# Kernel optimization log

Measured on AMD Instinct MI355X. Metric: run time of the kernel, lower is better.

Reference implementation:

```python
import jax, jax.numpy as jnp
import numpy as np

B, T, D, H = 4, 1024, 1024, 16
DS, DC, EXP = 16, 4, 2
DI = EXP * D            # 2048 inner SSM dim
DTR = D // 16           # 64 dt rank
K = max(1, int(0.2 * T))  # top-k tokens routed to attention
HD = D // H


def setup_inputs() -> dict:
    key = jax.random.key(0)
    ks = jax.random.split(key, 12)
    s = 0.02
    w = lambda k, shp: jax.random.normal(k, shp, jnp.float32) * s
    return {
        "x": jax.random.normal(ks[0], (B, T, D), jnp.float32),
        "ln_gamma": jnp.ones((D,), jnp.float32),
        "ln_beta": jnp.zeros((D,), jnp.float32),
        "Wr1": w(ks[1], (D, D // 4)), "br1": jnp.zeros((D // 4,), jnp.float32),
        "Wr2": w(ks[2], (D // 4, 1)), "br2": jnp.zeros((1,), jnp.float32),
        "Wqkv": w(ks[3], (D, 3 * D)), "bqkv": jnp.zeros((3 * D,), jnp.float32),
        "Wo": w(ks[4], (D, D)), "bo": jnp.zeros((D,), jnp.float32),
        "W_in": w(ks[5], (D, 2 * DI)),
        "conv_w": w(ks[6], (DI, DC)), "conv_b": jnp.zeros((DI,), jnp.float32),
        "W_xproj": w(ks[7], (DI, DTR + 2 * DS)),
        "W_dt": w(ks[8], (DTR, DI)), "b_dt": jnp.zeros((DI,), jnp.float32),
        "A_log": jnp.log(jnp.broadcast_to(jnp.arange(1, DS + 1, dtype=jnp.float32), (DI, DS))),
        "Dskip": jnp.ones((DI,), jnp.float32),
        "W_out": w(ks[9], (DI, D)),
    }


def _layernorm(x, g, b):
    mu = x.mean(-1, keepdims=True)
    v = ((x - mu) ** 2).mean(-1, keepdims=True)
    return (x - mu) * jax.lax.rsqrt(v + 1e-5) * g + b


def _attn(tok, Wqkv, bqkv, Wo, bo):
    # full MHA over the k selected tokens only: tok (B,K,D)
    qkv = tok @ Wqkv + bqkv
    q, k_, v = jnp.split(qkv, 3, axis=-1)
    q = q.reshape(B, K, H, HD).transpose(0, 2, 1, 3)   # bhkd
    k_ = k_.reshape(B, K, H, HD).transpose(0, 2, 1, 3)
    v = v.reshape(B, K, H, HD).transpose(0, 2, 1, 3)
    scores = jnp.einsum('bhqd,bhkd->bhqk', q, k_) / jnp.sqrt(jnp.float32(HD))
    p = jax.nn.softmax(scores, axis=-1)
    o = jnp.einsum('bhqk,bhkd->bhqd', p, v)
    o = o.transpose(0, 2, 1, 3).reshape(B, K, D)
    return o @ Wo + bo


def _ssm(xn, W_in, conv_w, conv_b, W_xproj, W_dt, b_dt, A_log, Dskip, W_out):
    # Mamba-style selective SSM over all tokens
    u, z = jnp.split(xn @ W_in, 2, axis=-1)            # (B,T,DI) each
    up = jnp.pad(u, ((0, 0), (DC - 1, 0), (0, 0)))      # causal depthwise conv
    uc = sum(up[:, j:j + T, :] * conv_w[:, j] for j in range(DC)) + conv_b
    u = jax.nn.silu(uc)
    proj = u @ W_xproj                                  # (B,T,DTR+2*DS)
    dt = jax.nn.softplus(proj[..., :DTR] @ W_dt + b_dt)  # (B,T,DI)
    Bm = proj[..., DTR:DTR + DS]                        # (B,T,DS)
    Cm = proj[..., DTR + DS:]                           # (B,T,DS)
    A = -jnp.exp(A_log)                                 # (DI,DS)
    dA = jnp.exp(dt[..., None] * A)                     # (B,T,DI,DS)
    dBu = dt[..., None] * Bm[:, :, None, :] * u[..., None]

    def step(h, inp):
        dA_t, dBu_t, C_t = inp
        h = dA_t * h + dBu_t                            # (B,DI,DS)
        y = (h * C_t[:, None, :]).sum(-1)               # (B,DI)
        return h, y

    h0 = jnp.zeros((B, DI, DS), dA.dtype)
    _, ys = jax.lax.scan(step, h0, (dA.transpose(1, 0, 2, 3),
                                    dBu.transpose(1, 0, 2, 3),
                                    Cm.transpose(1, 0, 2)))
    y = ys.transpose(1, 0, 2) + u * Dskip               # (B,T,DI)
    y = y * jax.nn.silu(z)
    return y @ W_out


def reference(x, ln_gamma, ln_beta, Wr1, br1, Wr2, br2, Wqkv, bqkv, Wo, bo,
              W_in, conv_w, conv_b, W_xproj, W_dt, b_dt, A_log, Dskip, W_out):
    xn = _layernorm(x, ln_gamma, ln_beta)
    scores = (jax.nn.relu(xn @ Wr1 + br1) @ Wr2 + br2)[..., 0]   # (B,T)
    _, idx = jax.lax.top_k(scores, K)                            # (B,K)
    bidx = jnp.arange(B)[:, None]
    mask = jnp.zeros((B, T), bool).at[bidx, idx].set(True)
    delta_ssm = _ssm(xn, W_in, conv_w, conv_b, W_xproj, W_dt, b_dt, A_log, Dskip, W_out)
    tok = xn[bidx, idx]                                          # gather (B,K,D)
    delta_tok = _attn(tok, Wqkv, bqkv, Wo, bo)
    delta_attn = jnp.zeros_like(xn).at[bidx, idx].set(delta_tok)  # scatter back
    delta = jnp.where(mask[..., None], delta_attn, delta_ssm)
    return x + delta
```

## Files before the change

kernel.cpp:

```cpp
#include <hip/hip_runtime.h>
#include <hip/hip_bf16.h>
#include <math.h>

#define BB   4
#define TT   1024
#define DD   1024
#define HH   16
#define DII  2048
#define DSS  16
#define DCC  4
#define KK   204
#define HDD  64
#define DTRR 64
#define NCH  32
#define LCH  32
#define KSPL 8
#define XPN  96
#define PRJ  128
#define RZ   8
#define RKC  3072
#define MPAD 896
#define WOZ  4

typedef short bf16x8 __attribute__((ext_vector_type(8)));
typedef short bf16x4v __attribute__((ext_vector_type(4)));
typedef float f32x4 __attribute__((ext_vector_type(4)));

#define GLDS16(g, l) __builtin_amdgcn_global_load_lds(                        \
    (const __attribute__((address_space(1))) void*)(g),                       \
    (__attribute__((address_space(3))) void*)(l), 16, 0, 0)

__device__ __forceinline__ ushort f2bu(float v) {
  __hip_bfloat16 h = __float2bfloat16(v);
  return __builtin_bit_cast(ushort, h);
}
__device__ __forceinline__ float b2f(ushort u) {
  __hip_bfloat16 h = __builtin_bit_cast(__hip_bfloat16, u);
  return __bfloat162float(h);
}

__device__ __forceinline__ float wave_sum(float v) {
#pragma unroll
  for (int o = 32; o > 0; o >>= 1) v += __shfl_xor(v, o, 64);
  return v;
}
__device__ __forceinline__ float block_sum256(float v, volatile float* sh) {
  v = wave_sum(v);
  if ((threadIdx.x & 63) == 0) sh[threadIdx.x >> 6] = v;
  __syncthreads();
  float r = sh[0] + sh[1] + sh[2] + sh[3];
  __syncthreads();
  return r;
}

__global__ __launch_bounds__(256) void layernorm_kernel(
    const float* __restrict__ x, const float* __restrict__ g,
    const float* __restrict__ be, ushort* __restrict__ xcat) {
  __shared__ float sh[4];
  int row = blockIdx.x;
  const float* xr = x + (size_t)row * DD;
  float v[4];
  float s = 0.f;
#pragma unroll
  for (int i = 0; i < 4; i++) { v[i] = xr[threadIdx.x + 256 * i]; s += v[i]; }
  float mean = block_sum256(s, sh) * (1.f / DD);
  float q = 0.f;
#pragma unroll
  for (int i = 0; i < 4; i++) { float d = v[i] - mean; q += d * d; }
  float var = block_sum256(q, sh) * (1.f / DD);
  float rstd = rsqrtf(var + 1e-5f);
  ushort* xc = xcat + (size_t)row * RKC;
#pragma unroll
  for (int i = 0; i < 4; i++) {
    int c = threadIdx.x + 256 * i;
    float o = (v[i] - mean) * rstd * g[c] + be[c];
    ushort hi = f2bu(o);
    float lo = o - b2f(hi);
    xc[c] = hi;
    xc[1024 + c] = hi;
    xc[2048 + c] = f2bu(lo);
  }
}

__device__ __forceinline__ void tile_transpose(
    const float* W, int rows, int cols, ushort* WT, int bx, int by,
    float tile[32][33]) {
  int c0 = bx * 32, r0 = by * 32;
  int tx = threadIdx.x & 31, ty = threadIdx.x >> 5;
#pragma unroll
  for (int i = 0; i < 32; i += 8)
    tile[ty + i][tx] = W[(size_t)(r0 + ty + i) * cols + c0 + tx];
  __syncthreads();
#pragma unroll
  for (int i = 0; i < 32; i += 8)
    WT[(size_t)(c0 + ty + i) * rows + r0 + tx] = f2bu(tile[tx][ty + i]);
}

__global__ __launch_bounds__(256) void transpose_all(
    const float* __restrict__ W_in, const float* __restrict__ W_out,
    const float* __restrict__ Wqkv, const float* __restrict__ Wo,
    const float* __restrict__ W_dt, const float* __restrict__ W_xproj,
    ushort* __restrict__ WinT, ushort* __restrict__ WoutT,
    ushort* __restrict__ WqkvT, ushort* __restrict__ WoT,
    ushort* __restrict__ WdtT, ushort* __restrict__ WxprojT) {
  __shared__ float tile[32][33];
  int lin = blockIdx.x;
  if (lin < 4096) {
    tile_transpose(W_in, 1024, 4096, WinT, lin % 128, lin / 128, tile);
  } else if ((lin -= 4096) < 2048) {
    tile_transpose(W_out, 2048, 1024, WoutT, lin % 32, lin / 32, tile);
  } else if ((lin -= 2048) < 3072) {
    tile_transpose(Wqkv, 1024, 3072, WqkvT, lin % 96, lin / 96, tile);
  } else if ((lin -= 3072) < 1024) {
    tile_transpose(Wo, 1024, 1024, WoT, lin % 32, lin / 32, tile);
  } else if ((lin -= 1024) < 128) {
    tile_transpose(W_dt, 64, 2048, WdtT, lin % 64, lin / 64, tile);
  } else {
    lin -= 128;
    tile_transpose(W_xproj, 2048, 96, WxprojT, lin % 3, lin / 3, tile);
  }
}

__global__ __launch_bounds__(256) void transpose_hilo(
    const float* __restrict__ W, ushort* __restrict__ WT) {
  __shared__ float tile[32][33];
  int c0 = blockIdx.x * 32, r0 = blockIdx.y * 32;
  int tx = threadIdx.x & 31, ty = threadIdx.x >> 5;
#pragma unroll
  for (int i = 0; i < 32; i += 8)
    tile[ty + i][tx] = W[(size_t)(r0 + ty + i) * 256 + c0 + tx];
  __syncthreads();
#pragma unroll
  for (int i = 0; i < 32; i += 8) {
    float v = tile[tx][ty + i];
    ushort hi = f2bu(v);
    float lo = v - b2f(hi);
    size_t base = (size_t)(c0 + ty + i) * RKC;
    WT[base + r0 + tx] = hi;
    WT[base + 1024 + r0 + tx] = f2bu(lo);
    WT[base + 2048 + r0 + tx] = hi;
  }
}

__global__ __launch_bounds__(512) void gemm_bf16_256(
    const ushort* __restrict__ A, int lda,
    const ushort* __restrict__ BT, int ldbt,
    void* __restrict__ Cv, int ldc, int K,
    const float* __restrict__ bias, const float* __restrict__ addmat,
    int outBf16) {
  __shared__ ushort Alds[256 * 64];
  __shared__ ushort Blds[256 * 64];
  int t = threadIdx.x;
  int wv = t >> 6, lane = t & 63;
  int wvm = wv >> 2, wvn = wv & 3;
  int nwg = gridDim.x * gridDim.y;
  int lin = blockIdx.y * gridDim.x + blockIdx.x;
  int swz = (lin & 7) * (nwg >> 3) + (lin >> 3);
  int bx = swz % gridDim.x, by = swz / gridDim.x;
  int row0 = by * 256, col0 = bx * 256;
  f32x4 acc[8][4] = {};

  const ushort* Ap[4];
  const ushort* Bp[4];
  ushort* Alb[4];
  ushort* Blb[4];
#pragma unroll
  for (int j = 0; j < 4; j++) {
    int c = j * 512 + t;
    int r = c >> 3;
    int kc = (((c & 7) ^ (r & 7)) * 8);
    Ap[j] = A + (size_t)(row0 + r) * lda + kc;
    Bp[j] = BT + (size_t)(col0 + r) * ldbt + kc;
    int cst = j * 512 + wv * 64;
    Alb[j] = Alds + (size_t)cst * 8;
    Blb[j] = Blds + (size_t)cst * 8;
  }
  int frow = lane & 15, fk = (lane >> 4) * 8;

  for (int k0 = 0; k0 < K; k0 += 64) {
#pragma unroll
    for (int j = 0; j < 4; j++) {
      GLDS16(Ap[j] + k0, Alb[j]);
      GLDS16(Bp[j] + k0, Blb[j]);
    }
    __syncthreads();
#pragma unroll
    for (int ks = 0; ks < 2; ks++) {
      bf16x8 af[8], bfv[4];
#pragma unroll
      for (int m = 0; m < 8; m++) {
        int row = wvm * 128 + m * 16 + frow;
        af[m] = *(const bf16x8*)&Alds[row * 64 +
                                      ((ks * 32 + fk) ^ ((row & 7) * 8))];
      }
#pragma unroll
      for (int n = 0; n < 4; n++) {
        int row = wvn * 64 + n * 16 + frow;
        bfv[n] = *(const bf16x8*)&Blds[row * 64 +
                                       ((ks * 32 + fk) ^ ((row & 7) * 8))];
      }
#pragma unroll
      for (int m = 0; m < 8; m++)
#pragma unroll
        for (int n = 0; n < 4; n++)
          acc[m][n] = __builtin_amdgcn_mfma_f32_16x16x32_bf16(af[m], bfv[n],
                                                              acc[m][n], 0, 0, 0);
    }
    __syncthreads();
  }
  int rbase = row0 + wvm * 128 + (lane >> 4) * 4;
  int cbase = col0 + wvn * 64 + (lane & 15);
  if (outBf16) {
    ushort* myL = Alds + wv * 1088;
    ushort* C16 = (ushort*)Cv;
    for (int m = 0; m < 8; m++) {
      __syncthreads();
#pragma unroll
      for (int n = 0; n < 4; n++) {
        int cc = cbase + n * 16;
        float bi = bias ? bias[cc] : 0.f;
#pragma unroll
        for (int i = 0; i < 4; i++)
          myL[((lane >> 4) * 4 + i) * 68 + (lane & 15) + n * 16] =
              f2bu(acc[m][n][i] + bi);
      }
      __syncthreads();
      int rr = lane >> 2, cg = lane & 3;
      bf16x8 v0 = *(const bf16x8*)&myL[rr * 68 + cg * 16];
      bf16x8 v1 = *(const bf16x8*)&myL[rr * 68 + cg * 16 + 8];
      size_t grow = (size_t)(row0 + wvm * 128 + m * 16 + rr) * ldc +
                    col0 + wvn * 64 + cg * 16;
      *(bf16x8*)&C16[grow] = v0;
      *(bf16x8*)&C16[grow + 8] = v1;
    }
  } else {
    float* C = (float*)Cv;
#pragma unroll
    for (int n = 0; n < 4; n++) {
      int cc = cbase + n * 16;
      float bi = bias ? bias[cc] : 0.f;
#pragma unroll
      for (int m = 0; m < 8; m++) {
#pragma unroll
        for (int i = 0; i < 4; i++) {
          size_t r = rbase + m * 16 + i;
          float v = acc[m][n][i] + bi;
          if (addmat) v += addmat[r * ldc + cc];
          C[r * ldc + cc] = v;
        }
      }
    }
  }
}

__global__ __launch_bounds__(512) void gemm_bf16_128x8(
    const ushort* __restrict__ A, int lda,
    const ushort* __restrict__ BT, int ldbt,
    void* __restrict__ Cv, int ldc, int K,
    const float* __restrict__ bias, const float* __restrict__ addmat,
    int act, int outBf16) {
  __shared__ ushort Alds[128 * 64];
  __shared__ ushort Blds[128 * 64];
  int t = threadIdx.x;
  int wv = t >> 6, lane = t & 63;
  int wvm = wv >> 1, wvn = wv & 1;
  int nwg = gridDim.x * gridDim.y;
  int lin = blockIdx.y * gridDim.x + blockIdx.x;
  int swz = (lin & 7) * (nwg >> 3) + (lin >> 3);
  int bx = swz % gridDim.x, by = swz / gridDim.x;
  int row0 = by * 128, col0 = bx * 128;
  f32x4 acc[2][4] = {};

  const ushort* Ap[2];
  const ushort* Bp[2];
  ushort* Alb[2];
  ushort* Blb[2];
#pragma unroll
  for (int j = 0; j < 2; j++) {
    int c = j * 512 + t;
    int r = c >> 3;
    int kc = (((c & 7) ^ (r & 7)) * 8);
    Ap[j] = A + (size_t)(row0 + r) * lda + kc;
    Bp[j] = BT + (size_t)(col0 + r) * ldbt + kc;
    int cst = j * 512 + wv * 64;
    Alb[j] = Alds + (size_t)cst * 8;
    Blb[j] = Blds + (size_t)cst * 8;
  }
  int frow = lane & 15, fk = (lane >> 4) * 8;

  for (int k0 = 0; k0 < K; k0 += 64) {
#pragma unroll
    for (int j = 0; j < 2; j++) {
      GLDS16(Ap[j] + k0, Alb[j]);
      GLDS16(Bp[j] + k0, Blb[j]);
    }
    __syncthreads();
#pragma unroll
    for (int ks = 0; ks < 2; ks++) {
      bf16x8 af[2], bfv[4];
#pragma unroll
      for (int m = 0; m < 2; m++) {
        int row = wvm * 32 + m * 16 + frow;
        af[m] = *(const bf16x8*)&Alds[row * 64 +
                                      ((ks * 32 + fk) ^ ((row & 7) * 8))];
      }
#pragma unroll
      for (int n = 0; n < 4; n++) {
        int row = wvn * 64 + n * 16 + frow;
        bfv[n] = *(const bf16x8*)&Blds[row * 64 +
                                       ((ks * 32 + fk) ^ ((row & 7) * 8))];
      }
#pragma unroll
      for (int m = 0; m < 2; m++)
#pragma unroll
        for (int n = 0; n < 4; n++)
          acc[m][n] = __builtin_amdgcn_mfma_f32_16x16x32_bf16(af[m], bfv[n],
                                                              acc[m][n], 0, 0, 0);
    }
    __syncthreads();
  }
  int rbase = row0 + wvm * 32 + (lane >> 4) * 4;
  int cbase = col0 + wvn * 64 + (lane & 15);
#pragma unroll
  for (int n = 0; n < 4; n++) {
    int cc = cbase + n * 16;
    float bi = bias ? bias[cc] : 0.f;
#pragma unroll
    for (int m = 0; m < 2; m++) {
#pragma unroll
      for (int i = 0; i < 4; i++) {
        size_t r = rbase + m * 16 + i;
        float v = acc[m][n][i] + bi;
        if (act == 2) v = (v > 20.f) ? v : log1pf(__expf(v));
        if (outBf16) {
          ((ushort*)Cv)[r * ldc + cc] = f2bu(v);
        } else {
          if (addmat) v += addmat[r * ldc + cc];
          ((float*)Cv)[r * ldc + cc] = v;
        }
      }
    }
  }
}

__global__ __launch_bounds__(512) void gemm_bf16_128x8_splitk(
    const ushort* __restrict__ A, int lda,
    const ushort* __restrict__ BT, int ldbt,
    float* __restrict__ partial, int ldc, int Ktot, size_t zstride) {
  __shared__ ushort Alds[128 * 64];
  __shared__ ushort Blds[128 * 64];
  int t = threadIdx.x;
  int wv = t >> 6, lane = t & 63;
  int wvm = wv >> 1, wvn = wv & 1;
  int nwg = gridDim.x * gridDim.y;
  int lin = blockIdx.y * gridDim.x + blockIdx.x;
  int swz = (lin & 7) * (nwg >> 3) + (lin >> 3);
  int bx = swz % gridDim.x, by = swz / gridDim.x;
  int row0 = by * 128, col0 = bx * 128;
  int kchunk = Ktot / gridDim.z;
  int kbeg = blockIdx.z * kchunk, kend = kbeg + kchunk;
  f32x4 acc[2][4] = {};

  const ushort* Ap[2];
  const ushort* Bp[2];
  ushort* Alb[2];
  ushort* Blb[2];
#pragma unroll
  for (int j = 0; j < 2; j++) {
    int c = j * 512 + t;
    int r = c >> 3;
    int kc = (((c & 7) ^ (r & 7)) * 8);
    Ap[j] = A + (size_t)(row0 + r) * lda + kc;
    Bp[j] = BT + (size_t)(col0 + r) * ldbt + kc;
    int cst = j * 512 + wv * 64;
    Alb[j] = Alds + (size_t)cst * 8;
    Blb[j] = Blds + (size_t)cst * 8;
  }
  int frow = lane & 15, fk = (lane >> 4) * 8;

  for (int k0 = kbeg; k0 < kend; k0 += 64) {
#pragma unroll
    for (int j = 0; j < 2; j++) {
      GLDS16(Ap[j] + k0, Alb[j]);
      GLDS16(Bp[j] + k0, Blb[j]);
    }
    __syncthreads();
#pragma unroll
    for (int ks = 0; ks < 2; ks++) {
      bf16x8 af[2], bfv[4];
#pragma unroll
      for (int m = 0; m < 2; m++) {
        int row = wvm * 32 + m * 16 + frow;
        af[m] = *(const bf16x8*)&Alds[row * 64 +
                                      ((ks * 32 + fk) ^ ((row & 7) * 8))];
      }
#pragma unroll
      for (int n = 0; n < 4; n++) {
        int row = wvn * 64 + n * 16 + frow;
        bfv[n] = *(const bf16x8*)&Blds[row * 64 +
                                       ((ks * 32 + fk) ^ ((row & 7) * 8))];
      }
#pragma unroll
      for (int m = 0; m < 2; m++)
#pragma unroll
        for (int n = 0; n < 4; n++)
          acc[m][n] = __builtin_amdgcn_mfma_f32_16x16x32_bf16(af[m], bfv[n],
                                                              acc[m][n], 0, 0, 0);
    }
    __syncthreads();
  }
  float* P = partial + (size_t)blockIdx.z * zstride;
  int rbase = row0 + wvm * 32 + (lane >> 4) * 4;
  int cbase = col0 + wvn * 64 + (lane & 15);
#pragma unroll
  for (int n = 0; n < 4; n++) {
    int cc = cbase + n * 16;
#pragma unroll
    for (int m = 0; m < 2; m++)
#pragma unroll
      for (int i = 0; i < 4; i++)
        P[(size_t)(rbase + m * 16 + i) * ldc + cc] = acc[m][n][i];
  }
}

__global__ __launch_bounds__(256) void router_score_reduce(
    const float* __restrict__ rpart, const float* __restrict__ br1,
    const float* __restrict__ Wr2, const float* __restrict__ br2,
    float* __restrict__ scores, size_t zstride) {
  __shared__ float sh[4];
  int row = blockIdx.x, c = threadIdx.x;
  size_t idx = (size_t)row * 256 + c;
  float s = 0.f;
#pragma unroll
  for (int z = 0; z < RZ; z++) s += rpart[z * zstride + idx];
  s = fmaxf(s + br1[c], 0.f);
  float tot = block_sum256(s * Wr2[c], sh);
  if (c == 0) scores[row] = tot + br2[0];
}

__global__ __launch_bounds__(256) void wo_scatter_reduce(
    const float* __restrict__ wpart, const float* __restrict__ x,
    const float* __restrict__ bo, const int* __restrict__ idx,
    float* __restrict__ out, size_t zstride) {
  int r = blockIdx.x;
  int b = r / KK;
  size_t orow = (size_t)(b * TT + idx[r]) * DD;
  int c4 = threadIdx.x * 4;
  f32x4 s = *(const f32x4*)&wpart[(size_t)r * DD + c4];
#pragma unroll
  for (int z = 1; z < WOZ; z++) {
    f32x4 p = *(const f32x4*)&wpart[z * zstride + (size_t)r * DD + c4];
#pragma unroll
    for (int j = 0; j < 4; j++) s[j] += p[j];
  }
  f32x4 xv = *(const f32x4*)&x[orow + c4];
  f32x4 bv = *(const f32x4*)&bo[c4];
#pragma unroll
  for (int j = 0; j < 4; j++) s[j] += xv[j] + bv[j];
  *(f32x4*)&out[orow + c4] = s;
}

__global__ __launch_bounds__(1024) void topk_kernel(
    const float* __restrict__ scores, int* __restrict__ idx) {
  __shared__ float s[1024];
  __shared__ int si[1024];
  int b = blockIdx.x, t = threadIdx.x;
  s[t] = scores[b * TT + t];
  si[t] = t;
  __syncthreads();
  for (int k = 2; k <= 1024; k <<= 1) {
    for (int j = k >> 1; j > 0; j >>= 1) {
      int partner = t ^ j;
      if (partner > t) {
        bool dirDesc = ((t & k) == 0);
        float s1 = s[t], s2 = s[partner];
        int i1 = si[t], i2 = si[partner];
        bool firstGreater = (s1 > s2) || (s1 == s2 && i1 < i2);
        bool doSwap = dirDesc ? !firstGreater : firstGreater;
        if (doSwap) { s[t] = s2; s[partner] = s1; si[t] = i2; si[partner] = i1; }
      }
      __syncthreads();
    }
  }
  if (t < KK) idx[b * KK + t] = si[t];
}

__global__ __launch_bounds__(256) void splitk_reduce_dual(
    const float* __restrict__ partial, float* __restrict__ C,
    __hip_bfloat16* __restrict__ Cb, int MN) {
  int i = blockIdx.x * 256 + threadIdx.x;
  if (i >= MN) return;
  float s = 0.f;
#pragma unroll
  for (int k = 0; k < KSPL; k++) s += partial[(size_t)k * MN + i];
  C[i] = s;
  Cb[i] = __float2bfloat16(s);
}

__global__ __launch_bounds__(256) void conv_silu_kernel(
    const ushort* __restrict__ uz, const float* __restrict__ conv_w,
    const float* __restrict__ conv_b, ushort* __restrict__ ub16) {
  size_t gid4 = ((size_t)blockIdx.x * 256 + threadIdx.x) * 4;
  int c = gid4 % DII;
  size_t bt = gid4 / DII;
  int t = bt % TT;
  int b = bt / TT;
  f32x4 cw[4];
#pragma unroll
  for (int ci = 0; ci < 4; ci++) cw[ci] = *(const f32x4*)&conv_w[(c + ci) * DCC];
  f32x4 sum = *(const f32x4*)&conv_b[c];
#pragma unroll
  for (int j = 0; j < DCC; j++) {
    int tt = t - (DCC - 1) + j;
    if (tt >= 0) {
      bf16x4v uv = *(const bf16x4v*)&uz[((size_t)(b * TT + tt)) * (2 * DII) + c];
#pragma unroll
      for (int ci = 0; ci < 4; ci++) sum[ci] += b2f((ushort)uv[ci]) * cw[ci][j];
    }
  }
  bf16x4v rb;
#pragma unroll
  for (int ci = 0; ci < 4; ci++)
    rb[ci] = (short)f2bu(sum[ci] / (1.f + __expf(-sum[ci])));
  *(bf16x4v*)&ub16[gid4] = rb;
}

__global__ __launch_bounds__(256) void ssm_phase1(
    const ushort* __restrict__ dt, const float* __restrict__ proj,
    const ushort* __restrict__ u, const float* __restrict__ A_log,
    float* __restrict__ hloc, float* __restrict__ Pprod) {
  int gid = blockIdx.x * 256 + threadIdx.x;
  int half = gid & 1;
  int cc = gid >> 1;
  int di = cc % DII;
  int rem = cc / DII;
  int chunk = rem % NCH;
  int b = rem / NCH;
  float a[8], h[8], P[8];
#pragma unroll
  for (int i = 0; i < 2; i++) {
    f32x4 al = *(const f32x4*)&A_log[di * DSS + half * 8 + i * 4];
#pragma unroll
    for (int j = 0; j < 4; j++) a[i * 4 + j] = -__expf(al[j]);
  }
#pragma unroll
  for (int s = 0; s < 8; s++) { h[s] = 0.f; P[s] = 1.f; }
  int t0 = chunk * LCH;
  for (int lt = 0; lt < LCH; lt++) {
    size_t bt = (size_t)(b * TT + t0 + lt);
    float dtv = b2f(dt[bt * DII + di]);
    float uv = b2f(u[bt * DII + di]);
    const float* pr = proj + bt * PRJ + DTRR + half * 8;
    float dtu = dtv * uv;
#pragma unroll
    for (int s = 0; s < 8; s++) {
      float dA = __expf(dtv * a[s]);
      h[s] = dA * h[s] + dtu * pr[s];
      P[s] *= dA;
    }
  }
#pragma unroll
  for (int i = 0; i < 2; i++) {
    *(f32x4*)&hloc[(size_t)cc * 16 + half * 8 + i * 4] = *(f32x4*)&h[i * 4];
    *(f32x4*)&Pprod[(size_t)cc * 16 + half * 8 + i * 4] = *(f32x4*)&P[i * 4];
  }
}

__global__ __launch_bounds__(256) void ssm_phase2(
    const float* __restrict__ hloc, const float* __restrict__ Pprod,
    float* __restrict__ hin) {
  int gid = blockIdx.x * 256 + threadIdx.x;
  int s_di = gid % (DII * 16);
  int b = gid / (DII * 16);
  float run = 0.f;
#pragma unroll
  for (int c = 0; c < NCH; c++) {
    size_t off = ((size_t)(b * NCH + c) * DII) * 16 + s_di;
    hin[off] = run;
    run = Pprod[off] * run + hloc[off];
  }
}

__global__ __launch_bounds__(256) void ssm_phase3(
    const ushort* __restrict__ dt, const float* __restrict__ proj,
    const ushort* __restrict__ u, const ushort* __restrict__ uz,
    const float* __restrict__ A_log, const float* __restrict__ Dskip,
    const float* __restrict__ hin, __hip_bfloat16* __restrict__ y) {
  int gid = blockIdx.x * 256 + threadIdx.x;
  int half = gid & 1;
  int cc = gid >> 1;
  int di = cc % DII;
  int rem = cc / DII;
  int chunk = rem % NCH;
  int b = rem / NCH;
  float a[8], h[8];
#pragma unroll
  for (int i = 0; i < 2; i++) {
    f32x4 al = *(const f32x4*)&A_log[di * DSS + half * 8 + i * 4];
    f32x4 hl = *(const f32x4*)&hin[(size_t)cc * 16 + half * 8 + i * 4];
#pragma unroll
    for (int j = 0; j < 4; j++) { a[i * 4 + j] = -__expf(al[j]); h[i * 4 + j] = hl[j]; }
  }
  float dsk = Dskip[di];
  int t0 = chunk * LCH;
  for (int lt = 0; lt < LCH; lt++) {
    size_t bt = (size_t)(b * TT + t0 + lt);
    float dtv = b2f(dt[bt * DII + di]);
    float uv = b2f(u[bt * DII + di]);
    const float* prB = proj + bt * PRJ + DTRR + half * 8;
    const float* prC = prB + DSS;
    float dtu = dtv * uv;
    float yp = 0.f;
#pragma unroll
    for (int s = 0; s < 8; s++) {
      float dA = __expf(dtv * a[s]);
      h[s] = dA * h[s] + dtu * prB[s];
      yp += h[s] * prC[s];
    }
    yp += __shfl_xor(yp, 1, 64);
    if (half == 0) {
      float zv = b2f(uz[bt * (2 * DII) + DII + di]);
      float sz = zv / (1.f + __expf(-zv));
      y[bt * DII + di] = __float2bfloat16((yp + uv * dsk) * sz);
    }
  }
}

__global__ __launch_bounds__(256) void gather_tok(
    const ushort* __restrict__ xcat, const int* __restrict__ idx,
    ushort* __restrict__ tok) {
  int r = blockIdx.x;
  int b = r / KK;
  int tsel = idx[r];
  const ushort* src = xcat + (size_t)(b * TT + tsel) * RKC;
  ushort* dst = tok + (size_t)r * DD;
#pragma unroll
  for (int j = 0; j < 4; j++) dst[threadIdx.x + 256 * j] = src[threadIdx.x + 256 * j];
}

#define KP 72
#define VP 232
__global__ __launch_bounds__(832) void attn_mfma_kernel(
    const ushort* __restrict__ qkv, ushort* __restrict__ attn_o) {
  __shared__ ushort Klds[208 * KP];
  __shared__ ushort VTlds[64 * VP];
  __shared__ ushort Plds[13 * 16 * VP];
  int bh = blockIdx.x;
  int h = bh % HH, b = bh / HH;
  int t = threadIdx.x;
  const ushort* base = qkv + (size_t)(b * KK) * 3072 + h * 64;

  for (int i = t; i < 208 * 64; i += 832) {
    int r = i >> 6, d = i & 63;
    Klds[r * KP + d] = (r < KK) ? base[(size_t)r * 3072 + 1024 + d] : (ushort)0;
  }
  for (int i = t; i < 208 * 64; i += 832) {
    int r = i >> 6, d = i & 63;
    VTlds[d * VP + r] = (r < KK) ? base[(size_t)r * 3072 + 2048 + d] : (ushort)0;
  }
  for (int i = t; i < 64 * (VP - 208); i += 832) {
    int d = i / (VP - 208), k = 208 + i % (VP - 208);
    VTlds[d * VP + k] = 0;
  }

  int wv = t >> 6, lane = t & 63;
  int q0 = wv * 16;
  int qrow = q0 + (lane & 15);
  if (qrow > KK - 1) qrow = KK - 1;
  const ushort* qptr = base + (size_t)qrow * 3072 + ((lane >> 4) * 8);
  bf16x8 qf[2];
#pragma unroll
  for (int ks = 0; ks < 2; ks++) qf[ks] = *(const bf16x8*)(qptr + ks * 32);
  ushort* myP = Plds + wv * 16 * VP;
  for (int i = lane; i < 16 * (VP - 208); i += 64) {
    int r = i / (VP - 208), k = 208 + i % (VP - 208);
    myP[r * VP + k] = 0;
  }
  __syncthreads();

  f32x4 sacc[13] = {};
#pragma unroll
  for (int nt = 0; nt < 13; nt++) {
#pragma unroll
    for (int ks = 0; ks < 2; ks++) {
      bf16x8 kf = *(const bf16x8*)&Klds[(nt * 16 + (lane & 15)) * KP +
                                        ks * 32 + (lane >> 4) * 8];
      sacc[nt] = __builtin_amdgcn_mfma_f32_16x16x32_bf16(qf[ks], kf, sacc[nt], 0, 0, 0);
    }
#pragma unroll
    for (int i = 0; i < 4; i++) sacc[nt][i] *= 0.125f;
  }
  if ((lane & 15) >= 12) {
#pragma unroll
    for (int i = 0; i < 4; i++) sacc[12][i] = -1e30f;
  }
  float m4[4], l4[4];
#pragma unroll
  for (int i = 0; i < 4; i++) {
    float m = sacc[0][i];
#pragma unroll
    for (int nt = 1; nt < 13; nt++) m = fmaxf(m, sacc[nt][i]);
    m = fmaxf(m, __shfl_xor(m, 1, 64));
    m = fmaxf(m, __shfl_xor(m, 2, 64));
    m = fmaxf(m, __shfl_xor(m, 4, 64));
    m = fmaxf(m, __shfl_xor(m, 8, 64));
    m4[i] = m;
  }
#pragma unroll
  for (int i = 0; i < 4; i++) {
    float ls = 0.f;
    int prow = (lane >> 4) * 4 + i;
#pragma unroll
    for (int nt = 0; nt < 13; nt++) {
      float e = __expf(sacc[nt][i] - m4[i]);
      ls += e;
      myP[prow * VP + nt * 16 + (lane & 15)] = f2bu(e);
    }
    ls += __shfl_xor(ls, 1, 64);
    ls += __shfl_xor(ls, 2, 64);
    ls += __shfl_xor(ls, 4, 64);
    ls += __shfl_xor(ls, 8, 64);
    l4[i] = ls;
  }
  f32x4 oacc[4] = {};
#pragma unroll
  for (int dt = 0; dt < 4; dt++) {
#pragma unroll
    for (int ks = 0; ks < 7; ks++) {
      bf16x8 pf = *(const bf16x8*)&myP[(lane & 15) * VP + ks * 32 + (lane >> 4) * 8];
      bf16x8 vf = *(const bf16x8*)&VTlds[(dt * 16 + (lane & 15)) * VP +
                                         ks * 32 + (lane >> 4) * 8];
      oacc[dt] = __builtin_amdgcn_mfma_f32_16x16x32_bf16(pf, vf, oacc[dt], 0, 0, 0);
    }
  }
#pragma unroll
  for (int i = 0; i < 4; i++) {
    int row = q0 + (lane >> 4) * 4 + i;
    if (row >= KK) continue;
    float inv = 1.f / l4[i];
#pragma unroll
    for (int dt = 0; dt < 4; dt++) {
      int col = dt * 16 + (lane & 15);
      attn_o[((size_t)(b * KK + row)) * DD + h * 64 + col] =
          f2bu(oacc[dt][i] * inv);
    }
  }
}

extern "C" void kernel_launch(void* const* d_in, const int* in_sizes, int n_in,
                              void* d_out, int out_size, void* d_ws, size_t ws_size,
                              hipStream_t stream) {
  const float* x = (const float*)d_in[0];
  const float* ln_g = (const float*)d_in[1];
  const float* ln_b = (const float*)d_in[2];
  const float* Wr1 = (const float*)d_in[3];
  const float* br1 = (const float*)d_in[4];
  const float* Wr2 = (const float*)d_in[5];
  const float* br2 = (const float*)d_in[6];
  const float* Wqkv = (const float*)d_in[7];
  const float* bqkv = (const float*)d_in[8];
  const float* Wo = (const float*)d_in[9];
  const float* bo = (const float*)d_in[10];
  const float* W_in = (const float*)d_in[11];
  const float* conv_w = (const float*)d_in[12];
  const float* conv_b = (const float*)d_in[13];
  const float* W_xproj = (const float*)d_in[14];
  const float* W_dt = (const float*)d_in[15];
  const float* b_dt = (const float*)d_in[16];
  const float* A_log = (const float*)d_in[17];
  const float* Dskip = (const float*)d_in[18];
  const float* W_out = (const float*)d_in[19];
  float* out = (float*)d_out;

  float* w = (float*)d_ws;
  size_t o = 0;
  float* scores = w + o; o += (size_t)BB * TT;
  int* idxb = (int*)(w + o); o += 1024;
  ushort* uzb16 = (ushort*)(w + o); o += (size_t)BB * TT * 2 * DII / 2;
  float* projb = w + o;  o += (size_t)BB * TT * PRJ;
  ushort* qkvb16 = (ushort*)(w + o); o += (size_t)MPAD * 3 * DD / 2 + 8;
  float* hloc = w + o;   o += (size_t)BB * NCH * DII * 16;
  float* Pprod = w + o;  o += (size_t)BB * NCH * DII * 16;
  float* hin = w + o;    o += (size_t)BB * NCH * DII * 16;
  ushort* xcat = (ushort*)(w + o);                  o += (size_t)BB * TT * RKC / 2;
  __hip_bfloat16* yb16 = (__hip_bfloat16*)(w + o);  o += (size_t)BB * TT * DII / 2;
  ushort* ub16 = (ushort*)(w + o);                  o += (size_t)BB * TT * DII / 2;
  ushort* dtb16 = (ushort*)(w + o);                 o += (size_t)BB * TT * DII / 2;
  ushort* tokb = (ushort*)(w + o);                  o += (size_t)MPAD * DD / 2 + 8;
  ushort* attno = (ushort*)(w + o);                 o += (size_t)MPAD * DD / 2 + 8;
  __hip_bfloat16* projb16 = (__hip_bfloat16*)(w + o); o += (size_t)BB * TT * PRJ / 2 + 8;
  ushort* Wr1cat = (ushort*)(w + o);                o += (size_t)256 * RKC / 2;
  ushort* WinT = (ushort*)(w + o);                  o += (size_t)(2 * DII) * DD / 2;
  ushort* WoutT = (ushort*)(w + o);                 o += (size_t)DD * DII / 2;
  ushort* WqkvT = (ushort*)(w + o);                 o += (size_t)(3 * DD) * DD / 2;
  ushort* WoT = (ushort*)(w + o);                   o += (size_t)DD * DD / 2;
  ushort* WdtT = (ushort*)(w + o);                  o += (size_t)DII * DTRR / 2;
  ushort* WxprojT = (ushort*)(w + o);               o += (size_t)PRJ * DII / 2;
  float* rpart = (float*)uzb16;
  float* xpart = hloc;
  float* wpart = hloc;
  const size_t RZSTR = (size_t)BB * TT * 256;
  const size_t XZSTR = (size_t)BB * TT * PRJ;
  const size_t WZSTR = (size_t)MPAD * DD;

  layernorm_kernel<<<BB * TT, 256, 0, stream>>>(x, ln_g, ln_b, xcat);
  transpose_all<<<10560, 256, 0, stream>>>(W_in, W_out, Wqkv, Wo, W_dt, W_xproj,
                                           WinT, WoutT, WqkvT, WoT, WdtT, WxprojT);
  transpose_hilo<<<dim3(256 / 32, DD / 32), 256, 0, stream>>>(Wr1, Wr1cat);
  gemm_bf16_128x8_splitk<<<dim3(256 / 128, BB * TT / 128, RZ), 512, 0, stream>>>(
      xcat, RKC, Wr1cat, RKC, rpart, 256, RKC, RZSTR);
  router_score_reduce<<<BB * TT, 256, 0, stream>>>(rpart, br1, Wr2, br2, scores,
                                                   RZSTR);
  topk_kernel<<<BB, 1024, 0, stream>>>(scores, idxb);
  gemm_bf16_256<<<dim3(2 * DII / 256, BB * TT / 256), 512, 0, stream>>>(
      xcat, RKC, WinT, DD, uzb16, 2 * DII, DD, nullptr, nullptr, 1);
  conv_silu_kernel<<<(BB * TT * DII) / 1024, 256, 0, stream>>>(uzb16, conv_w,
                                                               conv_b, ub16);
  gemm_bf16_128x8_splitk<<<dim3(PRJ / 128, BB * TT / 128, KSPL), 512, 0, stream>>>(
      ub16, DII, WxprojT, DII, xpart, PRJ, DII, XZSTR);
  splitk_reduce_dual<<<(int)((XZSTR + 255) / 256), 256, 0, stream>>>(
      xpart, projb, projb16, (int)XZSTR);
  gemm_bf16_128x8<<<dim3(DII / 128, BB * TT / 128), 512, 0, stream>>>(
      (const ushort*)projb16, PRJ, WdtT, DTRR, dtb16, DII, DTRR,
      b_dt, nullptr, 2, 1);
  ssm_phase1<<<(BB * NCH * DII * 2) / 256, 256, 0, stream>>>(dtb16, projb, ub16,
                                                             A_log, hloc, Pprod);
  ssm_phase2<<<(BB * DII * 16) / 256, 256, 0, stream>>>(hloc, Pprod, hin);
  ssm_phase3<<<(BB * NCH * DII * 2) / 256, 256, 0, stream>>>(dtb16, projb, ub16,
                                                             uzb16, A_log, Dskip,
                                                             hin, yb16);
  gemm_bf16_128x8<<<dim3(DD / 128, BB * TT / 128), 512, 0, stream>>>(
      (const ushort*)yb16, DII, WoutT, DII, out, DD, DII,
      nullptr, x, 0, 0);
  gather_tok<<<BB * KK, 256, 0, stream>>>(xcat, idxb, tokb);
  gemm_bf16_128x8<<<dim3(3 * DD / 128, MPAD / 128), 512, 0, stream>>>(
      tokb, DD, WqkvT, DD, qkvb16, 3 * DD, DD, bqkv, nullptr, 0, 1);
  attn_mfma_kernel<<<BB * HH, 832, 0, stream>>>(qkvb16, attno);
  gemm_bf16_128x8_splitk<<<dim3(DD / 128, MPAD / 128, WOZ), 512, 0, stream>>>(
      attno, DD, WoT, DD, wpart, DD, DD, WZSTR);
  wo_scatter_reduce<<<BB * KK, 256, 0, stream>>>(wpart, x, bo, idxb, out, WZSTR);
}
```

Before: 381.3 us.

## Overlap global-to-LDS loads with MFMA compute in bf16 GEMM kernels

The large-tile GEMM now keeps a single LDS buffer but issues the next tile's global-to-LDS loads after the second k-slice fragments are in registers, so the copy overlaps the second half of the MFMAs. The 128x8 and split-k GEMMs gain a double-buffered LDS ping-pong, prefetching tile k+1 while computing tile k. The aim is to hide global memory latency behind matrix math. The cost is doubled LDS use in the smaller kernels, which may lower occupancy, and more register pressure.

```diff
diff --git a/kernel.cpp b/kernel.cpp
--- a/kernel.cpp
+++ b/kernel.cpp
@@ -176,38 +176,61 @@
     Blb[j] = Blds + (size_t)cst * 8;
   }
   int frow = lane & 15, fk = (lane >> 4) * 8;
-
-  for (int k0 = 0; k0 < K; k0 += 64) {
-#pragma unroll
-    for (int j = 0; j < 4; j++) {
-      GLDS16(Ap[j] + k0, Alb[j]);
-      GLDS16(Bp[j] + k0, Blb[j]);
+  int nt = K / 64;
+
+#pragma unroll
+  for (int j = 0; j < 4; j++) {
+    GLDS16(Ap[j], Alb[j]);
+    GLDS16(Bp[j], Blb[j]);
+  }
+  __syncthreads();
+
+  for (int kt = 0; kt < nt; kt++) {
+    bf16x8 af[8], bfv[4];
+#pragma unroll
+    for (int m = 0; m < 8; m++) {
+      int row = wvm * 128 + m * 16 + frow;
+      af[m] = *(const bf16x8*)&Alds[row * 64 + (fk ^ ((row & 7) * 8))];
+    }
+#pragma unroll
+    for (int n = 0; n < 4; n++) {
+      int row = wvn * 64 + n * 16 + frow;
+      bfv[n] = *(const bf16x8*)&Blds[row * 64 + (fk ^ ((row & 7) * 8))];
+    }
+#pragma unroll
+    for (int m = 0; m < 8; m++)
+#pragma unroll
+      for (int n = 0; n < 4; n++)
+        acc[m][n] = __builtin_amdgcn_mfma_f32_16x16x32_bf16(af[m], bfv[n],
+                                                            acc[m][n], 0, 0, 0);
+#pragma unroll
+    for (int m = 0; m < 8; m++) {
+      int row = wvm * 128 + m * 16 + frow;
+      af[m] = *(const bf16x8*)&Alds[row * 64 + ((32 + fk) ^ ((row & 7) * 8))];
+    }
+#pragma unroll
+    for (int n = 0; n < 4; n++) {
+      int row = wvn * 64 + n * 16 + frow;
+      bfv[n] = *(const bf16x8*)&Blds[row * 64 + ((32 + fk) ^ ((row & 7) * 8))];
     }
     __syncthreads();
-#pragma unroll
-    for (int ks = 0; ks < 2; ks++) {
-      bf16x8 af[8], bfv[4];
-#pragma unroll
-      for (int m = 0; m < 8; m++) {
-        int row = wvm * 128 + m * 16 + frow;
-        af[m] = *(const bf16x8*)&Alds[row * 64 +
-                                      ((ks * 32 + fk) ^ ((row & 7) * 8))];
-      }
-#pragma unroll
-      for (int n = 0; n < 4; n++) {
-        int row = wvn * 64 + n * 16 + frow;
-        bfv[n] = *(const bf16x8*)&Blds[row * 64 +
-                                       ((ks * 32 + fk) ^ ((row & 7) * 8))];
-      }
-#pragma unroll
-      for (int m = 0; m < 8; m++)
-#pragma unroll
-        for (int n = 0; n < 4; n++)
-          acc[m][n] = __builtin_amdgcn_mfma_f32_16x16x32_bf16(af[m], bfv[n],
-                                                              acc[m][n], 0, 0, 0);
-    }
+    if (kt + 1 < nt) {
+      int k1 = (kt + 1) * 64;
+#pragma unroll
+      for (int j = 0; j < 4; j++) {
+        GLDS16(Ap[j] + k1, Alb[j]);
+        GLDS16(Bp[j] + k1, Blb[j]);
+      }
+    }
+#pragma unroll
+    for (int m = 0; m < 8; m++)
+#pragma unroll
+      for (int n = 0; n < 4; n++)
+        acc[m][n] = __builtin_amdgcn_mfma_f32_16x16x32_bf16(af[m], bfv[n],
+                                                            acc[m][n], 0, 0, 0);
     __syncthreads();
   }
+
   int rbase = row0 + wvm * 128 + (lane >> 4) * 4;
   int cbase = col0 + wvn * 64 + (lane & 15);
   if (outBf16) {
@@ -259,8 +282,8 @@
     void* __restrict__ Cv, int ldc, int K,
     const float* __restrict__ bias, const float* __restrict__ addmat,
     int act, int outBf16) {
-  __shared__ ushort Alds[128 * 64];
-  __shared__ ushort Blds[128 * 64];
+  __shared__ ushort Alds[2][128 * 64];
+  __shared__ ushort Blds[2][128 * 64];
   int t = threadIdx.x;
   int wv = t >> 6, lane = t & 63;
   int wvm = wv >> 1, wvn = wv & 1;
@@ -273,8 +296,7 @@
 
   const ushort* Ap[2];
   const ushort* Bp[2];
-  ushort* Alb[2];
-  ushort* Blb[2];
+  int cst[2];
 #pragma unroll
   for (int j = 0; j < 2; j++) {
     int c = j * 512 + t;
@@ -282,33 +304,42 @@
     int kc = (((c & 7) ^ (r & 7)) * 8);
     Ap[j] = A + (size_t)(row0 + r) * lda + kc;
     Bp[j] = BT + (size_t)(col0 + r) * ldbt + kc;
-    int cst = j * 512 + wv * 64;
-    Alb[j] = Alds + (size_t)cst * 8;
-    Blb[j] = Blds + (size_t)cst * 8;
+    cst[j] = j * 512 + wv * 64;
   }
   int frow = lane & 15, fk = (lane >> 4) * 8;
-
-  for (int k0 = 0; k0 < K; k0 += 64) {
-#pragma unroll
-    for (int j = 0; j < 2; j++) {
-      GLDS16(Ap[j] + k0, Alb[j]);
-      GLDS16(Bp[j] + k0, Blb[j]);
-    }
-    __syncthreads();
+  int nt = K / 64;
+
+#pragma unroll
+  for (int j = 0; j < 2; j++) {
+    GLDS16(Ap[j], &Alds[0][(size_t)cst[j] * 8]);
+    GLDS16(Bp[j], &Blds[0][(size_t)cst[j] * 8]);
+  }
+  __syncthreads();
+
+  for (int kt = 0; kt < nt; kt++) {
+    int cur = kt & 1;
+    if (kt + 1 < nt) {
+      int k1 = (kt + 1) * 64;
+#pragma unroll
+      for (int j = 0; j < 2; j++) {
+        GLDS16(Ap[j] + k1, &Alds[cur ^ 1][(size_t)cst[j] * 8]);
+        GLDS16(Bp[j] + k1, &Blds[cur ^ 1][(size_t)cst[j] * 8]);
+      }
+    }
+    const ushort* Ab = Alds[cur];
+    const ushort* Bb = Blds[cur];
 #pragma unroll
     for (int ks = 0; ks < 2; ks++) {
       bf16x8 af[2], bfv[4];
 #pragma unroll
       for (int m = 0; m < 2; m++) {
         int row = wvm * 32 + m * 16 + frow;
-        af[m] = *(const bf16x8*)&Alds[row * 64 +
-                                      ((ks * 32 + fk) ^ ((row & 7) * 8))];
+        af[m] = *(const bf16x8*)&Ab[row * 64 + ((ks * 32 + fk) ^ ((row & 7) * 8))];
       }
 #pragma unroll
       for (int n = 0; n < 4; n++) {
         int row = wvn * 64 + n * 16 + frow;
-        bfv[n] = *(const bf16x8*)&Blds[row * 64 +
-                                       ((ks * 32 + fk) ^ ((row & 7) * 8))];
+        bfv[n] = *(const bf16x8*)&Bb[row * 64 + ((ks * 32 + fk) ^ ((row & 7) * 8))];
       }
 #pragma unroll
       for (int m = 0; m < 2; m++)
@@ -319,6 +350,7 @@
     }
     __syncthreads();
   }
+
   int rbase = row0 + wvm * 32 + (lane >> 4) * 4;
   int cbase = col0 + wvn * 64 + (lane & 15);
 #pragma unroll
@@ -347,8 +379,8 @@
     const ushort* __restrict__ A, int lda,
     const ushort* __restrict__ BT, int ldbt,
     float* __restrict__ partial, int ldc, int Ktot, size_t zstride) {
-  __shared__ ushort Alds[128 * 64];
-  __shared__ ushort Blds[128 * 64];
+  __shared__ ushort Alds[2][128 * 64];
+  __shared__ ushort Blds[2][128 * 64];
   int t = threadIdx.x;
   int wv = t >> 6, lane = t & 63;
   int wvm = wv >> 1, wvn = wv & 1;
@@ -358,47 +390,55 @@
   int bx = swz % gridDim.x, by = swz / gridDim.x;
   int row0 = by * 128, col0 = bx * 128;
   int kchunk = Ktot / gridDim.z;
-  int kbeg = blockIdx.z * kchunk, kend = kbeg + kchunk;
+  int kbeg = blockIdx.z * kchunk;
   f32x4 acc[2][4] = {};
 
   const ushort* Ap[2];
   const ushort* Bp[2];
-  ushort* Alb[2];
-  ushort* Blb[2];
+  int cst[2];
 #pragma unroll
   for (int j = 0; j < 2; j++) {
     int c = j * 512 + t;
     int r = c >> 3;
     int kc = (((c & 7) ^ (r & 7)) * 8);
-    Ap[j] = A + (size_t)(row0 + r) * lda + kc;
-    Bp[j] = BT + (size_t)(col0 + r) * ldbt + kc;
-    int cst = j * 512 + wv * 64;
-    Alb[j] = Alds + (size_t)cst * 8;
-    Blb[j] = Blds + (size_t)cst * 8;
+    Ap[j] = A + (size_t)(row0 + r) * lda + kc + kbeg;
+    Bp[j] = BT + (size_t)(col0 + r) * ldbt + kc + kbeg;
+    cst[j] = j * 512 + wv * 64;
   }
   int frow = lane & 15, fk = (lane >> 4) * 8;
-
-  for (int k0 = kbeg; k0 < kend; k0 += 64) {
-#pragma unroll
-    for (int j = 0; j < 2; j++) {
-      GLDS16(Ap[j] + k0, Alb[j]);
-      GLDS16(Bp[j] + k0, Blb[j]);
-    }
-    __syncthreads();
+  int nt = kchunk / 64;
+
+#pragma unroll
+  for (int j = 0; j < 2; j++) {
+    GLDS16(Ap[j], &Alds[0][(size_t)cst[j] * 8]);
+    GLDS16(Bp[j], &Blds[0][(size_t)cst[j] * 8]);
+  }
+  __syncthreads();
+
+  for (int kt = 0; kt < nt; kt++) {
+    int cur = kt & 1;
+    if (kt + 1 < nt) {
+      int k1 = (kt + 1) * 64;
+#pragma unroll
+      for (int j = 0; j < 2; j++) {
+        GLDS16(Ap[j] + k1, &Alds[cur ^ 1][(size_t)cst[j] * 8]);
+        GLDS16(Bp[j] + k1, &Blds[cur ^ 1][(size_t)cst[j] * 8]);
+      }
+    }
+    const ushort* Ab = Alds[cur];
+    const ushort* Bb = Blds[cur];
 #pragma unroll
     for (int ks = 0; ks < 2; ks++) {
       bf16x8 af[2], bfv[4];
 #pragma unroll
       for (int m = 0; m < 2; m++) {
         int row = wvm * 32 + m * 16 + frow;
-        af[m] = *(const bf16x8*)&Alds[row * 64 +
-                                      ((ks * 32 + fk) ^ ((row & 7) * 8))];
+        af[m] = *(const bf16x8*)&Ab[row * 64 + ((ks * 32 + fk) ^ ((row & 7) * 8))];
       }
 #pragma unroll
       for (int n = 0; n < 4; n++) {
         int row = wvn * 64 + n * 16 + frow;
-        bfv[n] = *(const bf16x8*)&Blds[row * 64 +
-                                       ((ks * 32 + fk) ^ ((row & 7) * 8))];
+        bfv[n] = *(const bf16x8*)&Bb[row * 64 + ((ks * 32 + fk) ^ ((row & 7) * 8))];
       }
 #pragma unroll
       for (int m = 0; m < 2; m++)
```

Result: no change. 379.5 us (-0.5%).
